# Kernel optimization log

Hardware: AMD Instinct MI355X
Metric: run time of the kernel (lower is better)

The kernel has to match this reference:

```python
import jax, jax.numpy as jnp
import numpy as np

B, N, F_IN, H, FO = 4, 2048, 256, 4, 64


def setup_inputs() -> dict:
    key = jax.random.key(0)
    k1, k2, k3, k4, k5 = jax.random.split(key, 5)
    x = jax.random.normal(k1, (B, N, F_IN), dtype=jnp.float32)
    # random 0/1 adjacency with self-loops so every row of softmax is finite
    adj = jax.random.randint(k2, (N, N), 0, 2).astype(jnp.float32)
    adj = jnp.maximum(adj, jnp.eye(N, dtype=jnp.float32))
    # parameters (xavier-uniform style)
    lim_w = float(np.sqrt(6.0 / (F_IN + H * FO)))
    W = jax.random.uniform(k3, (F_IN, H * FO), minval=-lim_w, maxval=lim_w, dtype=jnp.float32)
    lim_a = float(np.sqrt(6.0 / (H + FO)))
    a_src = jax.random.uniform(k4, (H, FO), minval=-lim_a, maxval=lim_a, dtype=jnp.float32)
    a_dst = jax.random.uniform(k5, (H, FO), minval=-lim_a, maxval=lim_a, dtype=jnp.float32)
    return {"x": x, "adj": adj, "W": W, "a_src": a_src, "a_dst": a_dst}


def reference(x, adj, W, a_src, a_dst):
    # h: (B, N, H, FO)
    h = (x @ W).reshape(B, N, H, FO)
    attn_src = jnp.einsum("bnhf,hf->bnh", h, a_src)  # (B,N,H)
    attn_dst = jnp.einsum("bnhf,hf->bnh", h, a_dst)  # (B,N,H)
    # scores[b,i,j,h] = src[b,i,h] + dst[b,j,h]
    scores = attn_src[:, :, None, :] + attn_dst[:, None, :, :]
    scores = jax.nn.leaky_relu(scores, negative_slope=0.2)
    mask = (adj == 0)[None, :, :, None]  # (1,N,N,1)
    scores = jnp.where(mask, -jnp.inf, scores)
    attn = jax.nn.softmax(scores, axis=2)  # softmax over neighbors j
    # dropout is identity in eval mode / p=0
    out = jnp.einsum("bijh,bjhf->bihf", attn, h)  # (B,N,H,FO)
    return out.reshape(B, N, H * FO)  # concat=True
```

## Files before the change

kernel.cpp:

```cpp
#include <hip/hip_runtime.h>
#include <hip/hip_bf16.h>
#include <math.h>

#define B 4
#define N 2048
#define FIN 256
#define H 4
#define FO 64
#define M (B*N)
#define HF (H*FO)

typedef __attribute__((ext_vector_type(8))) short short8;
typedef __attribute__((ext_vector_type(4))) float float4v;
typedef __attribute__((ext_vector_type(4))) int int4v;

#if __has_builtin(__builtin_amdgcn_exp2f)
#define EXP2(x) __builtin_amdgcn_exp2f(x)
#else
#define EXP2(x) exp2f(x)
#endif

static __device__ __forceinline__ unsigned int pk_rne(float a, float b) {
  unsigned int ua = __builtin_bit_cast(unsigned int, a);
  unsigned int ub = __builtin_bit_cast(unsigned int, b);
  ua += 0x7fffu + ((ua >> 16) & 1u);
  ub += 0x7fffu + ((ub >> 16) & 1u);
  return (ua >> 16) | (ub & 0xffff0000u);
}

static __device__ __forceinline__ unsigned int pk_trunc(float a, float b) {
#if __has_builtin(__builtin_amdgcn_perm)
  return __builtin_amdgcn_perm(__builtin_bit_cast(unsigned int, b),
                               __builtin_bit_cast(unsigned int, a), 0x07060302u);
#else
  return (__builtin_bit_cast(unsigned int, a) >> 16) |
         (__builtin_bit_cast(unsigned int, b) & 0xffff0000u);
#endif
}

static __device__ __forceinline__ void split_pair(float x0, float x1,
                                                  unsigned int& hi, unsigned int& lo) {
  unsigned int u0 = __builtin_bit_cast(unsigned int, x0);
  unsigned int u1 = __builtin_bit_cast(unsigned int, x1);
  hi = (u0 >> 16) | (u1 & 0xffff0000u);
  float h0 = __builtin_bit_cast(float, u0 & 0xffff0000u);
  float h1 = __builtin_bit_cast(float, u1 & 0xffff0000u);
  unsigned int l0 = __builtin_bit_cast(unsigned int, x0 - h0);
  unsigned int l1 = __builtin_bit_cast(unsigned int, x1 - h1);
  lo = (l0 >> 16) | (l1 & 0xffff0000u);
}

static __device__ __forceinline__ unsigned int fenc(float f) {
  unsigned int b = __builtin_bit_cast(unsigned int, f);
  return (b & 0x80000000u) ? ~b : (b | 0x80000000u);
}
static __device__ __forceinline__ float fdec(unsigned int e) {
  unsigned int b = (e & 0x80000000u) ? (e & 0x7fffffffu) : ~e;
  return __builtin_bit_cast(float, b);
}

__global__ __launch_bounds__(256) void prep_pack(const float* __restrict__ Wsrc,
                                                 const float* __restrict__ X,
                                                 const float* __restrict__ adj,
                                                 unsigned short* __restrict__ Wf_hi,
                                                 unsigned short* __restrict__ Wf_lo,
                                                 unsigned short* __restrict__ Xf_hi,
                                                 unsigned short* __restrict__ Xf_lo,
                                                 unsigned long long* __restrict__ packed,
                                                 unsigned int* __restrict__ DmaxEnc) {
  const int blk = blockIdx.x;
  const int t = threadIdx.x;
  if (blk >= 144) {
    const int row = blk - 144;
    const int w = t >> 6, l = t & 63;
    const float* ar = adj + (size_t)row * N;
    for (int c = w; c < N / 64; c += 4) {
      unsigned long long m = __ballot(ar[c * 64 + l] != 0.f);
      if (l == 0) packed[(size_t)row * (N / 64) + c] = m;
    }
    return;
  }
  __shared__ float lds[64][65];
  if (blk < 16) {
    if (blk == 0 && t < 16) DmaxEnc[t] = 0u;
    const int k0 = (blk >> 2) * 64;
    const int h  = blk & 3;
    const int n0 = h * 64;
    const int c4 = (t & 15) * 4;
    #pragma unroll
    for (int rep = 0; rep < 4; ++rep) {
      const int kl = (t >> 4) + 16 * rep;
      const float4 v = *(const float4*)(Wsrc + (size_t)(k0 + kl) * HF + n0 + c4);
      lds[kl][c4 + 0] = v.x; lds[kl][c4 + 1] = v.y;
      lds[kl][c4 + 2] = v.z; lds[kl][c4 + 3] = v.w;
    }
    __syncthreads();
    #pragma unroll
    for (int rep = 0; rep < 2; ++rep) {
      const int s   = t + rep * 256;
      const int kcl = s >> 8;
      const int tt  = (s >> 6) & 3;
      const int ln  = s & 63;
      const int fL  = tt * 16 + (ln & 15);
      const int kb  = kcl * 32 + (ln >> 4) * 8;
      unsigned int hv[4], lv[4];
      #pragma unroll
      for (int p = 0; p < 4; ++p)
        split_pair(lds[kb + 2 * p][fL], lds[kb + 2 * p + 1][fL], hv[p], lv[p]);
      const size_t off = ((((size_t)h * 8 + (k0 >> 5) + kcl) * 4 + tt) << 9) + ln * 8;
      *(uint4*)(Wf_hi + off) = make_uint4(hv[0], hv[1], hv[2], hv[3]);
      *(uint4*)(Wf_lo + off) = make_uint4(lv[0], lv[1], lv[2], lv[3]);
    }
    return;
  }
  const int xblk  = blk - 16;
  const int mrow0 = xblk * 64;
  for (int ktile = 0; ktile < 4; ++ktile) {
    if (ktile) __syncthreads();
    const int k0 = ktile * 64;
    const int c4 = (t & 15) * 4;
    #pragma unroll
    for (int rep = 0; rep < 4; ++rep) {
      const int rl = (t >> 4) + 16 * rep;
      const float4 v = *(const float4*)(X + (size_t)(mrow0 + rl) * FIN + k0 + c4);
      lds[rl][c4 + 0] = v.x; lds[rl][c4 + 1] = v.y;
      lds[rl][c4 + 2] = v.z; lds[rl][c4 + 3] = v.w;
    }
    __syncthreads();
    #pragma unroll
    for (int rep = 0; rep < 2; ++rep) {
      const int s   = t + rep * 256;
      const int mt  = s >> 7;
      const int kcl = (s >> 6) & 1;
      const int ln  = s & 63;
      const int mrl = mt * 16 + (ln & 15);
      const int kb  = kcl * 32 + (ln >> 4) * 8;
      unsigned int hv[4], lv[4];
      #pragma unroll
      for (int p = 0; p < 4; ++p)
        split_pair(lds[mrl][kb + 2 * p], lds[mrl][kb + 2 * p + 1], hv[p], lv[p]);
      const size_t off = (((size_t)(xblk * 4 + mt) * 8 + (ktile * 2 + kcl)) << 9) + ln * 8;
      *(uint4*)(Xf_hi + off) = make_uint4(hv[0], hv[1], hv[2], hv[3]);
      *(uint4*)(Xf_lo + off) = make_uint4(lv[0], lv[1], lv[2], lv[3]);
    }
  }
}

__global__ __launch_bounds__(256) void gemm_fused(const unsigned short* __restrict__ Xf_hi,
                                                  const unsigned short* __restrict__ Xf_lo,
                                                  const unsigned short* __restrict__ Wf_hi,
                                                  const unsigned short* __restrict__ Wf_lo,
                                                  const float* __restrict__ a_src,
                                                  const float* __restrict__ a_dst,
                                                  float* __restrict__ Srcv,
                                                  float2* __restrict__ Epair,
                                                  unsigned int* __restrict__ DmaxEnc,
                                                  unsigned short* __restrict__ Hf) {
  __shared__ unsigned short sh[64][72];
  __shared__ float smax[4];
  const int xcd  = blockIdx.x & 7;
  const int slot = blockIdx.x >> 3;
  const int mb = xcd * 16 + (slot >> 2);
  const int h  = slot & 3;
  const int w = threadIdx.x >> 6, lane = threadIdx.x & 63;
  const int fl = lane & 15, quad = lane >> 4;
  const float L2E = 1.4426950408889634f;

  const float4v zero = {0.f, 0.f, 0.f, 0.f};
  float4v acc[4] = {zero, zero, zero, zero};

  const size_t abase = (((size_t)(mb * 4 + w) * 8) << 9) + lane * 8;
  #pragma unroll
  for (int kc = 0; kc < 8; ++kc) {
    const short8 Ahi = *(const short8*)(Xf_hi + abase + ((size_t)kc << 9));
    const short8 Alo = *(const short8*)(Xf_lo + abase + ((size_t)kc << 9));
    #pragma unroll
    for (int t = 0; t < 4; ++t) {
      const size_t woff = ((((size_t)h * 8 + kc) * 4 + t) << 9) + lane * 8;
      const short8 Bhi = *(const short8*)(Wf_hi + woff);
      const short8 Blo = *(const short8*)(Wf_lo + woff);
      acc[t] = __builtin_amdgcn_mfma_f32_16x16x32_bf16(Ahi, Bhi, acc[t], 0, 0, 0);
      acc[t] = __builtin_amdgcn_mfma_f32_16x16x32_bf16(Alo, Bhi, acc[t], 0, 0, 0);
      acc[t] = __builtin_amdgcn_mfma_f32_16x16x32_bf16(Ahi, Blo, acc[t], 0, 0, 0);
    }
  }

  const int bb  = (mb * 64) >> 11;
  const int n0w = (mb * 64) & (N - 1);
  const int bh  = bb * H + h;
  float as[4], ad[4];
  #pragma unroll
  for (int t = 0; t < 4; ++t) {
    as[t] = a_src[h * FO + t * 16 + fl];
    ad[t] = a_dst[h * FO + t * 16 + fl];
  }
  float wmax = -INFINITY;
  #pragma unroll
  for (int reg = 0; reg < 4; ++reg) {
    float sv = 0.f, dv = 0.f;
    #pragma unroll
    for (int t = 0; t < 4; ++t) {
      sv = fmaf(acc[t][reg], as[t], sv);
      dv = fmaf(acc[t][reg], ad[t], dv);
    }
    #pragma unroll
    for (int off = 1; off <= 8; off <<= 1) {
      sv += __shfl_xor(sv, off, 64);
      dv += __shfl_xor(dv, off, 64);
    }
    wmax = fmaxf(wmax, dv);
    if (fl == 0) {
      const int node = n0w + w * 16 + quad * 4 + reg;
      Srcv[(bh << 11) + node] = sv;
      float2 e;
      e.x = EXP2(dv * L2E);
      e.y = EXP2(dv * (0.2f * L2E));
      Epair[(bh << 11) + node] = e;
    }
  }
  wmax = fmaxf(wmax, __shfl_xor(wmax, 16, 64));
  wmax = fmaxf(wmax, __shfl_xor(wmax, 32, 64));
  if (lane == 0) smax[w] = wmax;

  #pragma unroll
  for (int t = 0; t < 4; ++t) {
    const int nl = w * 16 + quad * 4;
    *(unsigned int*)&sh[t * 16 + fl][nl]     = pk_rne(acc[t][0], acc[t][1]);
    *(unsigned int*)&sh[t * 16 + fl][nl + 2] = pk_rne(acc[t][2], acc[t][3]);
  }
  __syncthreads();
  if (threadIdx.x == 0) {
    const float bmax = fmaxf(fmaxf(smax[0], smax[1]), fmaxf(smax[2], smax[3]));
    atomicMax(DmaxEnc + bh, fenc(bmax));
  }
  const int jc0 = n0w >> 5;
  #pragma unroll
  for (int rep = 0; rep < 2; ++rep) {
    const int s = (int)threadIdx.x + rep * 256;
    const int jcl = s >> 8;
    const int tt  = (s >> 6) & 3;
    const int ln  = s & 63;
    const int f    = tt * 16 + (ln & 15);
    const int node = jcl * 32 + (ln >> 4) * 8;
    unsigned short* dsth = Hf + (((size_t)bh * 64 + jc0 + jcl) * 4 + tt) * 512 + ln * 8;
    *(uint4*)dsth = *(const uint4*)&sh[f][node];
  }
}

__global__ __launch_bounds__(1024) void gat_mfma(const unsigned char* __restrict__ pb,
                                                 const float* __restrict__ Src,
                                                 const float2* __restrict__ Epair,
                                                 const unsigned int* __restrict__ DmaxEnc,
                                                 const unsigned short* __restrict__ Hf,
                                                 float* __restrict__ out) {
  const int xcd  = blockIdx.x & 7;
  const int slot = blockIdx.x >> 3;
  const int b    = xcd >> 1;
  const int i0   = ((xcd & 1) * 64 + slot) * 16;
  const int w    = threadIdx.x >> 6;
  const int lane = threadIdx.x & 63;
  const int h    = w & 3;
  const int q    = w >> 2;
  const int bh   = b * H + h;
  const int fl   = lane & 15;
  const int kk   = (lane >> 4) * 8;
  const float L2E = 1.4426950408889634f;

  const int row0 = i0 + fl;
  const float dmx = fdec(DmaxEnc[bh]);
  const float s0 = Src[(bh << 11) + row0];
  const float u0 = s0 + dmx, m0 = fmaxf(u0, 0.2f * u0);
  const float c1a = EXP2((s0 - m0) * L2E), c2a = EXP2((0.2f * s0 - m0) * L2E);
  const float ta = EXP2(-s0 * L2E);
  const float* ep = (const float*)(Epair + (bh << 11));
  const unsigned char* pb0 = pb + (size_t)row0 * (N / 8);
  const unsigned short* hfb = Hf + (size_t)bh * 64 * 2048 + lane * 8;

  const short onebf = 0x3F80;
  short8 ones;
  #pragma unroll
  for (int jj = 0; jj < 8; ++jj) ones[jj] = onebf;

  const float4v zero = {0.f, 0.f, 0.f, 0.f};
  float4v acc[4] = {zero, zero, zero, zero};
  float4v accL = zero;

  const int jbeg = q * (N / 4);
  #pragma unroll 2
  for (int j0 = jbeg; j0 < jbeg + N / 4; j0 += 32) {
    const unsigned short* hc = hfb + (size_t)(j0 >> 5) * 2048;
    const short8 b0 = *(const short8*)(hc + 0 * 512);
    const short8 b1 = *(const short8*)(hc + 1 * 512);
    const short8 b2 = *(const short8*)(hc + 2 * 512);
    const short8 b3 = *(const short8*)(hc + 3 * 512);
    const float4 q0 = *(const float4*)(ep + 2 * (j0 + kk) + 0);
    const float4 q1 = *(const float4*)(ep + 2 * (j0 + kk) + 4);
    const float4 q2 = *(const float4*)(ep + 2 * (j0 + kk) + 8);
    const float4 q3 = *(const float4*)(ep + 2 * (j0 + kk) + 12);
    const unsigned int mk0 = pb0[(j0 + kk) >> 3];
    const float E1v[8] = {q0.x, q0.z, q1.x, q1.z, q2.x, q2.z, q3.x, q3.z};
    const float E2v[8] = {q0.y, q0.w, q1.y, q1.w, q2.y, q2.w, q3.y, q3.w};
    int p0i[4];
    #pragma unroll
    for (int p = 0; p < 4; ++p) {
      const int e0 = 2 * p, e1 = 2 * p + 1;
      const bool sa0 = E1v[e0] > ta;
      float va0 = (sa0 ? c1a : c2a) * (sa0 ? E1v[e0] : E2v[e0]);
      va0 = ((mk0 >> e0) & 1u) ? va0 : 0.f;
      const bool sa1 = E1v[e1] > ta;
      float va1 = (sa1 ? c1a : c2a) * (sa1 ? E1v[e1] : E2v[e1]);
      va1 = ((mk0 >> e1) & 1u) ? va1 : 0.f;
      p0i[p] = (int)pk_trunc(va0, va1);
    }
    const short8 p0 = __builtin_bit_cast(short8, (int4v){p0i[0], p0i[1], p0i[2], p0i[3]});
    acc[0] = __builtin_amdgcn_mfma_f32_16x16x32_bf16(p0, b0, acc[0], 0, 0, 0);
    acc[1] = __builtin_amdgcn_mfma_f32_16x16x32_bf16(p0, b1, acc[1], 0, 0, 0);
    acc[2] = __builtin_amdgcn_mfma_f32_16x16x32_bf16(p0, b2, acc[2], 0, 0, 0);
    acc[3] = __builtin_amdgcn_mfma_f32_16x16x32_bf16(p0, b3, acc[3], 0, 0, 0);
    accL   = __builtin_amdgcn_mfma_f32_16x16x32_bf16(p0, ones, accL, 0, 0, 0);
  }

  __shared__ float4v parts[4][64][5];
  for (int r = 3; r >= 1; --r) {
    if (q == r) {
      #pragma unroll
      for (int t = 0; t < 4; ++t) parts[h][lane][t] = acc[t];
      parts[h][lane][4] = accL;
    }
    __syncthreads();
    if (q == r - 1) {
      #pragma unroll
      for (int t = 0; t < 4; ++t) acc[t] += parts[h][lane][t];
      accL += parts[h][lane][4];
    }
    __syncthreads();
  }

  if (q == 0) {
    const int quad = lane >> 4;
    #pragma unroll
    for (int reg = 0; reg < 4; ++reg) {
      const int r = i0 + quad * 4 + reg;
      const float invl = 1.f / accL[reg];
      float* op = out + ((size_t)(b * N) + r) * HF + h * FO + fl;
      #pragma unroll
      for (int t = 0; t < 4; ++t) op[t * 16] = acc[t][reg] * invl;
    }
  }
}

extern "C" void kernel_launch(void* const* d_in, const int* in_sizes, int n_in,
                              void* d_out, int out_size, void* d_ws, size_t ws_size,
                              hipStream_t stream) {
  const float* x     = (const float*)d_in[0];
  const float* adj   = (const float*)d_in[1];
  const float* W     = (const float*)d_in[2];
  const float* a_src = (const float*)d_in[3];
  const float* a_dst = (const float*)d_in[4];
  float* out = (float*)d_out;

  char* p = (char*)d_ws;
  float* Srcv = (float*)p;                 p += (size_t)B * H * N * 4;
  float2* Epair = (float2*)p;              p += (size_t)B * H * N * 8;
  unsigned int* DmaxEnc = (unsigned int*)p; p += 256;
  unsigned short* Wfh = (unsigned short*)p; p += (size_t)HF * FIN * 2;
  unsigned short* Wfl = (unsigned short*)p; p += (size_t)HF * FIN * 2;
  unsigned short* Xfh = (unsigned short*)p; p += (size_t)M * FIN * 2;
  unsigned short* Xfl = (unsigned short*)p; p += (size_t)M * FIN * 2;
  unsigned short* Hf  = (unsigned short*)p; p += (size_t)M * HF * 2;
  unsigned long long* packed = (unsigned long long*)p;

  prep_pack<<<dim3(144 + N), dim3(256), 0, stream>>>(W, x, adj, Wfh, Wfl, Xfh, Xfl,
                                                     packed, DmaxEnc);
  gemm_fused<<<dim3((M / 64) * H), dim3(256), 0, stream>>>(Xfh, Xfl, Wfh, Wfl,
                                                           a_src, a_dst,
                                                           Srcv, Epair, DmaxEnc, Hf);
  gat_mfma<<<dim3(B * (N / 16)), dim3(1024), 0, stream>>>((const unsigned char*)packed,
                                                          Srcv, Epair, DmaxEnc, Hf, out);
}
```

Before: 144.4 us.

## Process two 16-row tiles per wave to reuse H fragments, with register prefetch

Each block now covers 32 query rows with 512 threads. Every wave computes attention for two 16-row tiles and shares the loaded H and E fragments between them, with the j range split two ways instead of four. Next-iteration loads are software-prefetched into registers, and the shared-memory reduction drops to a single stage. This halves the global/L2 traffic for H and E per output row and cuts reduction syncs, at the cost of more registers per thread and fewer waves for hiding latency.

```diff
diff --git a/kernel.cpp b/kernel.cpp
--- a/kernel.cpp
+++ b/kernel.cpp
@@ -247,33 +247,38 @@
   }
 }
 
-__global__ __launch_bounds__(1024) void gat_mfma(const unsigned char* __restrict__ pb,
-                                                 const float* __restrict__ Src,
-                                                 const float2* __restrict__ Epair,
-                                                 const unsigned int* __restrict__ DmaxEnc,
-                                                 const unsigned short* __restrict__ Hf,
-                                                 float* __restrict__ out) {
+__global__ __launch_bounds__(512) void gat_mfma(const unsigned char* __restrict__ pb,
+                                                const float* __restrict__ Src,
+                                                const float2* __restrict__ Epair,
+                                                const unsigned int* __restrict__ DmaxEnc,
+                                                const unsigned short* __restrict__ Hf,
+                                                float* __restrict__ out) {
   const int xcd  = blockIdx.x & 7;
   const int slot = blockIdx.x >> 3;
   const int b    = xcd >> 1;
-  const int i0   = ((xcd & 1) * 64 + slot) * 16;
+  const int i0   = ((xcd & 1) * 32 + slot) * 32;
   const int w    = threadIdx.x >> 6;
   const int lane = threadIdx.x & 63;
   const int h    = w & 3;
-  const int q    = w >> 2;
+  const int jh   = w >> 2;
   const int bh   = b * H + h;
   const int fl   = lane & 15;
   const int kk   = (lane >> 4) * 8;
   const float L2E = 1.4426950408889634f;
 
   const int row0 = i0 + fl;
+  const int row1 = i0 + 16 + fl;
   const float dmx = fdec(DmaxEnc[bh]);
   const float s0 = Src[(bh << 11) + row0];
+  const float s1 = Src[(bh << 11) + row1];
   const float u0 = s0 + dmx, m0 = fmaxf(u0, 0.2f * u0);
+  const float u1 = s1 + dmx, m1 = fmaxf(u1, 0.2f * u1);
   const float c1a = EXP2((s0 - m0) * L2E), c2a = EXP2((0.2f * s0 - m0) * L2E);
-  const float ta = EXP2(-s0 * L2E);
+  const float c1b = EXP2((s1 - m1) * L2E), c2b = EXP2((0.2f * s1 - m1) * L2E);
+  const float ta = EXP2(-s0 * L2E), tb = EXP2(-s1 * L2E);
   const float* ep = (const float*)(Epair + (bh << 11));
   const unsigned char* pb0 = pb + (size_t)row0 * (N / 8);
+  const unsigned char* pb1 = pb + (size_t)row1 * (N / 8);
   const unsigned short* hfb = Hf + (size_t)bh * 64 * 2048 + lane * 8;
 
   const short onebf = 0x3F80;
@@ -282,25 +287,54 @@
   for (int jj = 0; jj < 8; ++jj) ones[jj] = onebf;
 
   const float4v zero = {0.f, 0.f, 0.f, 0.f};
-  float4v acc[4] = {zero, zero, zero, zero};
-  float4v accL = zero;
-
-  const int jbeg = q * (N / 4);
-  #pragma unroll 2
-  for (int j0 = jbeg; j0 < jbeg + N / 4; j0 += 32) {
-    const unsigned short* hc = hfb + (size_t)(j0 >> 5) * 2048;
-    const short8 b0 = *(const short8*)(hc + 0 * 512);
-    const short8 b1 = *(const short8*)(hc + 1 * 512);
-    const short8 b2 = *(const short8*)(hc + 2 * 512);
-    const short8 b3 = *(const short8*)(hc + 3 * 512);
-    const float4 q0 = *(const float4*)(ep + 2 * (j0 + kk) + 0);
-    const float4 q1 = *(const float4*)(ep + 2 * (j0 + kk) + 4);
-    const float4 q2 = *(const float4*)(ep + 2 * (j0 + kk) + 8);
-    const float4 q3 = *(const float4*)(ep + 2 * (j0 + kk) + 12);
-    const unsigned int mk0 = pb0[(j0 + kk) >> 3];
+  float4v acc[2][4];
+  float4v accL[2];
+  #pragma unroll
+  for (int rt = 0; rt < 2; ++rt) {
+    accL[rt] = zero;
+    #pragma unroll
+    for (int t = 0; t < 4; ++t) acc[rt][t] = zero;
+  }
+
+  const int jbeg = jh * (N / 2);
+  short8 nb0, nb1, nb2, nb3;
+  float4 nq0, nq1, nq2, nq3;
+  unsigned int nm0, nm1;
+  {
+    const unsigned short* hc = hfb + (size_t)(jbeg >> 5) * 2048;
+    nb0 = *(const short8*)(hc + 0 * 512);
+    nb1 = *(const short8*)(hc + 1 * 512);
+    nb2 = *(const short8*)(hc + 2 * 512);
+    nb3 = *(const short8*)(hc + 3 * 512);
+    nq0 = *(const float4*)(ep + 2 * (jbeg + kk) + 0);
+    nq1 = *(const float4*)(ep + 2 * (jbeg + kk) + 4);
+    nq2 = *(const float4*)(ep + 2 * (jbeg + kk) + 8);
+    nq3 = *(const float4*)(ep + 2 * (jbeg + kk) + 12);
+    nm0 = pb0[(jbeg + kk) >> 3];
+    nm1 = pb1[(jbeg + kk) >> 3];
+  }
+
+  for (int it = 0; it < 32; ++it) {
+    const short8 b0 = nb0, b1 = nb1, b2 = nb2, b3 = nb3;
+    const float4 q0 = nq0, q1 = nq1, q2 = nq2, q3 = nq3;
+    const unsigned int mk0 = nm0, mk1 = nm1;
+    if (it < 31) {
+      const int jn = jbeg + (it + 1) * 32;
+      const unsigned short* hc = hfb + (size_t)(jn >> 5) * 2048;
+      nb0 = *(const short8*)(hc + 0 * 512);
+      nb1 = *(const short8*)(hc + 1 * 512);
+      nb2 = *(const short8*)(hc + 2 * 512);
+      nb3 = *(const short8*)(hc + 3 * 512);
+      nq0 = *(const float4*)(ep + 2 * (jn + kk) + 0);
+      nq1 = *(const float4*)(ep + 2 * (jn + kk) + 4);
+      nq2 = *(const float4*)(ep + 2 * (jn + kk) + 8);
+      nq3 = *(const float4*)(ep + 2 * (jn + kk) + 12);
+      nm0 = pb0[(jn + kk) >> 3];
+      nm1 = pb1[(jn + kk) >> 3];
+    }
     const float E1v[8] = {q0.x, q0.z, q1.x, q1.z, q2.x, q2.z, q3.x, q3.z};
     const float E2v[8] = {q0.y, q0.w, q1.y, q1.w, q2.y, q2.w, q3.y, q3.w};
-    int p0i[4];
+    int p0i[4], p1i[4];
     #pragma unroll
     for (int p = 0; p < 4; ++p) {
       const int e0 = 2 * p, e1 = 2 * p + 1;
@@ -311,40 +345,56 @@
       float va1 = (sa1 ? c1a : c2a) * (sa1 ? E1v[e1] : E2v[e1]);
       va1 = ((mk0 >> e1) & 1u) ? va1 : 0.f;
       p0i[p] = (int)pk_trunc(va0, va1);
+      const bool sb0 = E1v[e0] > tb;
+      float vb0 = (sb0 ? c1b : c2b) * (sb0 ? E1v[e0] : E2v[e0]);
+      vb0 = ((mk1 >> e0) & 1u) ? vb0 : 0.f;
+      const bool sb1 = E1v[e1] > tb;
+      float vb1 = (sb1 ? c1b : c2b) * (sb1 ? E1v[e1] : E2v[e1]);
+      vb1 = ((mk1 >> e1) & 1u) ? vb1 : 0.f;
+      p1i[p] = (int)pk_trunc(vb0, vb1);
     }
     const short8 p0 = __builtin_bit_cast(short8, (int4v){p0i[0], p0i[1], p0i[2], p0i[3]});
-    acc[0] = __builtin_amdgcn_mfma_f32_16x16x32_bf16(p0, b0, acc[0], 0, 0, 0);
-    acc[1] = __builtin_amdgcn_mfma_f32_16x16x32_bf16(p0, b1, acc[1], 0, 0, 0);
-    acc[2] = __builtin_amdgcn_mfma_f32_16x16x32_bf16(p0, b2, acc[2], 0, 0, 0);
-    acc[3] = __builtin_amdgcn_mfma_f32_16x16x32_bf16(p0, b3, acc[3], 0, 0, 0);
-    accL   = __builtin_amdgcn_mfma_f32_16x16x32_bf16(p0, ones, accL, 0, 0, 0);
-  }
-
-  __shared__ float4v parts[4][64][5];
-  for (int r = 3; r >= 1; --r) {
-    if (q == r) {
+    const short8 p1 = __builtin_bit_cast(short8, (int4v){p1i[0], p1i[1], p1i[2], p1i[3]});
+    acc[0][0] = __builtin_amdgcn_mfma_f32_16x16x32_bf16(p0, b0, acc[0][0], 0, 0, 0);
+    acc[0][1] = __builtin_amdgcn_mfma_f32_16x16x32_bf16(p0, b1, acc[0][1], 0, 0, 0);
+    acc[0][2] = __builtin_amdgcn_mfma_f32_16x16x32_bf16(p0, b2, acc[0][2], 0, 0, 0);
+    acc[0][3] = __builtin_amdgcn_mfma_f32_16x16x32_bf16(p0, b3, acc[0][3], 0, 0, 0);
+    accL[0]   = __builtin_amdgcn_mfma_f32_16x16x32_bf16(p0, ones, accL[0], 0, 0, 0);
+    acc[1][0] = __builtin_amdgcn_mfma_f32_16x16x32_bf16(p1, b0, acc[1][0], 0, 0, 0);
+    acc[1][1] = __builtin_amdgcn_mfma_f32_16x16x32_bf16(p1, b1, acc[1][1], 0, 0, 0);
+    acc[1][2] = __builtin_amdgcn_mfma_f32_16x16x32_bf16(p1, b2, acc[1][2], 0, 0, 0);
+    acc[1][3] = __builtin_amdgcn_mfma_f32_16x16x32_bf16(p1, b3, acc[1][3], 0, 0, 0);
+    accL[1]   = __builtin_amdgcn_mfma_f32_16x16x32_bf16(p1, ones, accL[1], 0, 0, 0);
+  }
+
+  __shared__ float4v parts[4][64][11];
+  if (jh == 1) {
+    #pragma unroll
+    for (int rt = 0; rt < 2; ++rt) {
       #pragma unroll
-      for (int t = 0; t < 4; ++t) parts[h][lane][t] = acc[t];
-      parts[h][lane][4] = accL;
-    }
-    __syncthreads();
-    if (q == r - 1) {
+      for (int t = 0; t < 4; ++t) parts[h][lane][rt * 5 + t] = acc[rt][t];
+      parts[h][lane][rt * 5 + 4] = accL[rt];
+    }
+  }
+  __syncthreads();
+  if (jh == 0) {
+    #pragma unroll
+    for (int rt = 0; rt < 2; ++rt) {
       #pragma unroll
-      for (int t = 0; t < 4; ++t) acc[t] += parts[h][lane][t];
-      accL += parts[h][lane][4];
-    }
-    __syncthreads();
-  }
-
-  if (q == 0) {
+      for (int t = 0; t < 4; ++t) acc[rt][t] += parts[h][lane][rt * 5 + t];
+      accL[rt] += parts[h][lane][rt * 5 + 4];
+    }
     const int quad = lane >> 4;
     #pragma unroll
-    for (int reg = 0; reg < 4; ++reg) {
-      const int r = i0 + quad * 4 + reg;
-      const float invl = 1.f / accL[reg];
-      float* op = out + ((size_t)(b * N) + r) * HF + h * FO + fl;
+    for (int rt = 0; rt < 2; ++rt) {
       #pragma unroll
-      for (int t = 0; t < 4; ++t) op[t * 16] = acc[t][reg] * invl;
+      for (int reg = 0; reg < 4; ++reg) {
+        const int r = i0 + rt * 16 + quad * 4 + reg;
+        const float invl = 1.f / accL[rt][reg];
+        float* op = out + ((size_t)(b * N) + r) * HF + h * FO + fl;
+        #pragma unroll
+        for (int t = 0; t < 4; ++t) op[t * 16] = acc[rt][t][reg] * invl;
+      }
     }
   }
 }
@@ -375,6 +425,6 @@
   gemm_fused<<<dim3((M / 64) * H), dim3(256), 0, stream>>>(Xfh, Xfl, Wfh, Wfl,
                                                            a_src, a_dst,
                                                            Srcv, Epair, DmaxEnc, Hf);
-  gat_mfma<<<dim3(B * (N / 16)), dim3(1024), 0, stream>>>((const unsigned char*)packed,
-                                                          Srcv, Epair, DmaxEnc, Hf, out);
-}
+  gat_mfma<<<dim3(B * (N / 32)), dim3(512), 0, stream>>>((const unsigned char*)packed,
+                                                         Srcv, Epair, DmaxEnc, Hf, out);
+}
```

Result: faster. 131.0 us (-9.3%).
